# Kernel tuning notes

Hardware: AMD Instinct MI355X
Metric: run time of the kernel (lower is better)

The kernel has to match this reference:

```python
import jax, jax.numpy as jnp
import numpy as np

N = 50000      # nodes
E = 800000     # edges (avg degree 16)
DIN = 128
H = 128
DOUT = 64


def setup_inputs() -> dict:
    key = jax.random.key(0)
    ks = jax.random.split(key, 8)
    x = jax.random.normal(ks[0], (N, DIN), dtype=jnp.float32)
    edge_index = jax.random.randint(ks[1], (2, E), 0, N, dtype=jnp.int32)
    def glorot(k, fi, fo):
        return jax.random.normal(k, (fi, fo), dtype=jnp.float32) * (1.0 / np.sqrt(fi))
    return {
        "x": x,
        "edge_index": edge_index,
        "W1": glorot(ks[2], DIN, H), "b1": jnp.zeros((H,), jnp.float32),
        "W2": glorot(ks[3], H, H),   "b2": jnp.zeros((H,), jnp.float32),
        "W3": glorot(ks[4], H, DOUT),"b3": jnp.zeros((DOUT,), jnp.float32),
    }


def reference(x, edge_index, W1, b1, W2, b2, W3, b3):
    n = x.shape[0]
    # GCNConv: add self-loops, symmetric degree normalization D^-1/2 (A+I) D^-1/2
    loop = jnp.arange(n, dtype=edge_index.dtype)
    src = jnp.concatenate([edge_index[0], loop])  # [E+N]
    dst = jnp.concatenate([edge_index[1], loop])
    deg = jax.ops.segment_sum(jnp.ones(src.shape, x.dtype), dst, num_segments=n)
    dinv = jnp.where(deg > 0, jax.lax.rsqrt(deg), 0.0)
    norm = dinv[src] * dinv[dst]  # [E+N]

    def conv(h, W, b):
        h = h @ W                                   # [N, out]
        msg = h[src] * norm[:, None]                # gather + scale
        return jax.ops.segment_sum(msg, dst, num_segments=n) + b

    # gelu after every layer except the last (forward breaks before act)
    h = jax.nn.gelu(conv(x, W1, b1), approximate=False)
    h = jax.nn.gelu(conv(h, W2, b2), approximate=False)
    return conv(h, W3, b3)
```

## Files before the change

### kernel.cpp

```cpp
#include <hip/hip_runtime.h>
#include <math.h>

#define NDIN 128
#define NHID 128
#define NDOUT 64
#define NREP 8

typedef _Float16 half2_t __attribute__((ext_vector_type(2)));
typedef _Float16 half4_t __attribute__((ext_vector_type(4)));
typedef _Float16 half8_t __attribute__((ext_vector_type(8)));
typedef float    float4v __attribute__((ext_vector_type(4)));

__device__ __forceinline__ float gelu_exact(float x) {
    return 0.5f * x * (1.0f + erff(x * 0.70710678118654752f));
}


__device__ void wtrans_tile(const float* __restrict__ W, _Float16* __restrict__ Wt,
                            int K, int N, int bx, int by) {
    __shared__ float tile[32][33];
    int tx = threadIdx.x & 31, ty = threadIdx.x >> 5;
    for (int i = 0; i < 32; i += 8) {
        int k = by * 32 + ty + i, nn = bx * 32 + tx;
        tile[ty + i][tx] = (k < K && nn < N) ? W[(size_t)k * N + nn] : 0.f;
    }
    __syncthreads();
    for (int i = 0; i < 32; i += 8) {
        int nn = bx * 32 + ty + i, k = by * 32 + tx;
        if (nn < N && k < K) Wt[(size_t)nn * K + k] = (_Float16)tile[tx][ty + i];
    }
}

__global__ __launch_bounds__(256) void prep0_kernel(
    const float* __restrict__ W1, _Float16* __restrict__ W1t,
    const float* __restrict__ W2, _Float16* __restrict__ W2t,
    const float* __restrict__ W3, _Float16* __restrict__ W3t,
    int* __restrict__ countR, int* __restrict__ done, int n) {
    int b = blockIdx.x;
    if (b < 16) {
        wtrans_tile(W1, W1t, NDIN, NHID, b & 3, b >> 2);
    } else if (b < 32) {
        wtrans_tile(W2, W2t, NHID, NHID, (b - 16) & 3, (b - 16) >> 2);
    } else if (b < 40) {
        wtrans_tile(W3, W3t, NHID, NDOUT, (b - 32) & 1, (b - 32) >> 1);
    } else {
        int z = b - 40;
        int i = z * 256 + threadIdx.x;
        if (i < NREP * n) countR[i] = 0;
        if (z == 0 && threadIdx.x < 64) done[threadIdx.x] = 0;
    }
}


__global__ void count_kernel(const int* __restrict__ dst, int* __restrict__ countR,
                             int* __restrict__ eslot, int E, int n) {
    int b = blockIdx.x;
    int e = b * 256 + threadIdx.x;
    if (e < E) eslot[e] = atomicAdd(&countR[(b & (NREP - 1)) * n + dst[e]], 1);
}


__global__ __launch_bounds__(256) void reduce_scan_kernel(
    int* __restrict__ countR, int* __restrict__ blocksum, int* __restrict__ blockoff,
    int* __restrict__ rowptr, float* __restrict__ dinv, int* __restrict__ done,
    int nb, int n) {
    __shared__ int s[256];
    __shared__ int flag;
    __shared__ int boff_s;
    int t = threadIdx.x;
    int i = blockIdx.x * 256 + t;
    int deg = 0;
    if (i < n) {
        int pre = 0;
#pragma unroll
        for (int r = 0; r < NREP; r++) {
            int c = countR[r * n + i];
            countR[r * n + i] = pre;
            pre += c;
        }
        deg = pre;
    }
    s[t] = deg;
    __syncthreads();
    for (int off = 128; off > 0; off >>= 1) {
        if (t < off) s[t] += s[t + off];
        __syncthreads();
    }
    if (t == 0) {
        atomicExch(&blocksum[blockIdx.x], s[0]);
        __threadfence();
        int old = atomicAdd(&done[0], 1);
        flag = (old == nb - 1) ? 1 : 0;
    }
    __syncthreads();
    if (flag) {
        __threadfence();
        int pv = (t < nb) ? atomicAdd(&blocksum[t], 0) : 0;
        s[t] = pv;
        __syncthreads();
        for (int off = 1; off < 256; off <<= 1) {
            int u = (t >= off) ? s[t - off] : 0;
            __syncthreads();
            s[t] += u;
            __syncthreads();
        }
        if (t < nb) atomicExch(&blockoff[t], s[t] - pv);
        if (t == 255) rowptr[n] = s[255];
        __threadfence();
        if (t == 0) atomicExch(&done[1], 1);
    } else if (t == 0) {
        while (atomicAdd(&done[1], 0) == 0) __builtin_amdgcn_s_sleep(2);
        __threadfence();
    }
    __syncthreads();
    if (t == 0) boff_s = atomicAdd(&blockoff[blockIdx.x], 0);
    s[t] = deg;
    __syncthreads();
    for (int off = 1; off < 256; off <<= 1) {
        int u = (t >= off) ? s[t - off] : 0;
        __syncthreads();
        s[t] += u;
        __syncthreads();
    }
    if (i < n) {
        rowptr[i] = boff_s + s[t] - deg;
        dinv[i] = rsqrtf((float)(deg + 1));
    }
}


__global__ void fill_kernel(const int* __restrict__ src, const int* __restrict__ dst,
                            const int* __restrict__ eslot, const float* __restrict__ dinv,
                            const int* __restrict__ rowptr, const int* __restrict__ countR,
                            int2* __restrict__ adj, int E, int n) {
    int e = blockIdx.x * 256 + threadIdx.x;
    if (e >= E) return;
    int s = src[e], d = dst[e];
    int r = (e >> 8) & (NREP - 1);
    int p = rowptr[d] + countR[r * n + d] + eslot[e];
    adj[p] = make_int2(s, __float_as_int(dinv[s] * dinv[d]));
}


template <int BN, bool AF16>
__global__ __launch_bounds__(256) void gemm_mfma(
    const void* __restrict__ Aptr, const _Float16* __restrict__ Bt,
    _Float16* __restrict__ T, int M) {
    __shared__ _Float16 lds_a[64][136];
    __shared__ _Float16 lds_bt[BN][136];
    const int K = 128;
    int tid = threadIdx.x;
    int bm = blockIdx.x * 64;
    int wave = tid >> 6, lane = tid & 63;
    int m = lane & 15, quad = lane >> 4;

    if (AF16) {
        const _Float16* A = (const _Float16*)Aptr;
#pragma unroll
        for (int j = 0; j < 4; j++) {
            int c = tid + j * 256;
            int r = c >> 4, col = (c & 15) << 3;
            int grow = bm + r;
            uint4 v = make_uint4(0, 0, 0, 0);
            if (grow < M) v = *(const uint4*)(A + (size_t)grow * K + col);
            *(uint4*)&lds_a[r][col] = v;
        }
    } else {
        const float* A = (const float*)Aptr;
#pragma unroll
        for (int j = 0; j < 8; j++) {
            int c = tid + j * 256;
            int r = c >> 5, col = (c & 31) << 2;
            int grow = bm + r;
            float4 v = make_float4(0.f, 0.f, 0.f, 0.f);
            if (grow < M) v = *(const float4*)(A + (size_t)grow * K + col);
            half4_t h;
            h[0] = (_Float16)v.x; h[1] = (_Float16)v.y;
            h[2] = (_Float16)v.z; h[3] = (_Float16)v.w;
            *(half4_t*)&lds_a[r][col] = h;
        }
    }
    {
        const int chunks = BN * K / 8;
        for (int c = tid; c < chunks; c += 256) {
            int r = c >> 4, col = (c & 15) << 3;
            *(uint4*)&lds_bt[r][col] = *(const uint4*)(Bt + (size_t)r * K + col);
        }
    }
    __syncthreads();

    const int NT = BN / 16;
    float4v acc[NT];
#pragma unroll
    for (int nt = 0; nt < NT; nt++) acc[nt] = (float4v){0.f, 0.f, 0.f, 0.f};

    int arow = (wave << 4) + m;
#pragma unroll
    for (int kc = 0; kc < K; kc += 32) {
        half8_t a = *(const half8_t*)&lds_a[arow][kc + quad * 8];
#pragma unroll
        for (int nt = 0; nt < NT; nt++) {
            half8_t b = *(const half8_t*)&lds_bt[nt * 16 + m][kc + quad * 8];
            acc[nt] = __builtin_amdgcn_mfma_f32_16x16x32_f16(a, b, acc[nt], 0, 0, 0);
        }
    }
#pragma unroll
    for (int nt = 0; nt < NT; nt++) {
#pragma unroll
        for (int r = 0; r < 4; r++) {
            int grow = bm + (wave << 4) + (quad << 2) + r;
            if (grow < M) T[(size_t)grow * BN + nt * 16 + m] = (_Float16)acc[nt][r];
        }
    }
}


__device__ __forceinline__ half2_t agg_node128(
    const half2_t* __restrict__ t2, const int* __restrict__ rowptr,
    const int2* __restrict__ adj, const float* __restrict__ dinv,
    const float* __restrict__ bias, int node, int lane) {
    float wself = dinv[node];
    wself *= wself;
    half2_t v = t2[(size_t)node * 64 + lane];
    float accx = wself * (float)v[0], accy = wself * (float)v[1];
    int beg = rowptr[node], end = rowptr[node + 1];
    for (int e0 = beg; e0 < end; e0 += 64) {
        int rem = end - e0;
        int j = 0; float w = 0.f;
        if (lane < rem) {
            int2 ed = adj[e0 + lane];
            j = ed.x; w = __int_as_float(ed.y);
        }
        int cnt = rem < 64 ? rem : 64;
        for (int c = 0; c < cnt; c += 16) {
#pragma unroll
            for (int i = 0; i < 16; i++) {
                int jj = __builtin_amdgcn_readlane(j, c + i);
                float ww = __int_as_float(
                    __builtin_amdgcn_readlane(__float_as_int(w), c + i));
                half2_t u = t2[(size_t)jj * 64 + lane];
                accx += ww * (float)u[0];
                accy += ww * (float)u[1];
            }
        }
    }
    float2 b = ((const float2*)bias)[lane];
    accx = gelu_exact(accx + b.x);
    accy = gelu_exact(accy + b.y);
    half2_t o; o[0] = (_Float16)accx; o[1] = (_Float16)accy;
    return o;
}


template <int BN>
__global__ __launch_bounds__(256) void agg_gemm16_kernel(
    const _Float16* __restrict__ t, const int* __restrict__ rowptr,
    const int2* __restrict__ adj, const float* __restrict__ dinv,
    const float* __restrict__ bias, const _Float16* __restrict__ Bt,
    _Float16* __restrict__ T, int M) {
    __shared__ _Float16 lds_a[16][136];
    int tid = threadIdx.x;
    int wave = tid >> 6, lane = tid & 63;
    int bm = blockIdx.x * 16;
    const half2_t* t2 = (const half2_t*)t;
#pragma unroll 1
    for (int p = 0; p < 4; p++) {
        int r = (wave << 2) + p;
        int node = bm + r;
        half2_t o;
        o[0] = (_Float16)0.f; o[1] = (_Float16)0.f;
        if (node < M) o = agg_node128(t2, rowptr, adj, dinv, bias, node, lane);
        *(half2_t*)&lds_a[r][lane << 1] = o;
    }
    __syncthreads();

    int m = lane & 15, quad = lane >> 4;
    const int NT = BN / 64;
    float4v acc[NT];
#pragma unroll
    for (int nt = 0; nt < NT; nt++) acc[nt] = (float4v){0.f, 0.f, 0.f, 0.f};
#pragma unroll
    for (int kc = 0; kc < 128; kc += 32) {
        half8_t a = *(const half8_t*)&lds_a[m][kc + quad * 8];
#pragma unroll
        for (int nt = 0; nt < NT; nt++) {
            int col = wave * (BN / 4) + nt * 16 + m;
            half8_t b = *(const half8_t*)&Bt[(size_t)col * 128 + kc + quad * 8];
            acc[nt] = __builtin_amdgcn_mfma_f32_16x16x32_f16(a, b, acc[nt], 0, 0, 0);
        }
    }
#pragma unroll
    for (int nt = 0; nt < NT; nt++) {
#pragma unroll
        for (int r = 0; r < 4; r++) {
            int grow = bm + (quad << 2) + r;
            int col = wave * (BN / 4) + nt * 16 + m;
            if (grow < M) T[(size_t)grow * BN + col] = (_Float16)acc[nt][r];
        }
    }
}


template <int F, bool DOGELU, bool OUTF16>
__global__ __launch_bounds__(256) void agg_kernel(
    const _Float16* __restrict__ t, const int* __restrict__ rowptr,
    const int2* __restrict__ adj, const float* __restrict__ dinv,
    const float* __restrict__ bias, void* __restrict__ outp, int n) {
    int node = (int)((blockIdx.x * blockDim.x + threadIdx.x) >> 6);
    int lane = threadIdx.x & 63;
    if (node >= n) return;

    float wself = dinv[node];
    wself *= wself;
    int beg = rowptr[node];
    int end = rowptr[node + 1];

    if (F == 128) {
        const half2_t* t2 = (const half2_t*)t;
        half2_t v = t2[(size_t)node * 64 + lane];
        float accx = wself * (float)v[0], accy = wself * (float)v[1];
        for (int e0 = beg; e0 < end; e0 += 64) {
            int rem = end - e0;
            int j = 0; float w = 0.f;
            if (lane < rem) {
                int2 ed = adj[e0 + lane];
                j = ed.x; w = __int_as_float(ed.y);
            }
            int cnt = rem < 64 ? rem : 64;
            for (int c = 0; c < cnt; c += 16) {
#pragma unroll
                for (int i = 0; i < 16; i++) {
                    int jj = __builtin_amdgcn_readlane(j, c + i);
                    float ww = __int_as_float(
                        __builtin_amdgcn_readlane(__float_as_int(w), c + i));
                    half2_t u = t2[(size_t)jj * 64 + lane];
                    accx += ww * (float)u[0];
                    accy += ww * (float)u[1];
                }
            }
        }
        float2 b = ((const float2*)bias)[lane];
        accx += b.x; accy += b.y;
        if (DOGELU) { accx = gelu_exact(accx); accy = gelu_exact(accy); }
        if (OUTF16) {
            half2_t o; o[0] = (_Float16)accx; o[1] = (_Float16)accy;
            ((half2_t*)outp)[(size_t)node * 64 + lane] = o;
        } else {
            float2 o; o.x = accx; o.y = accy;
            ((float2*)outp)[(size_t)node * 64 + lane] = o;
        }
    } else {
        float acc = wself * (float)t[(size_t)node * 64 + lane];
        for (int e0 = beg; e0 < end; e0 += 64) {
            int rem = end - e0;
            int j = 0; float w = 0.f;
            if (lane < rem) {
                int2 ed = adj[e0 + lane];
                j = ed.x; w = __int_as_float(ed.y);
            }
            int cnt = rem < 64 ? rem : 64;
            for (int c = 0; c < cnt; c += 16) {
#pragma unroll
                for (int i = 0; i < 16; i++) {
                    int jj = __builtin_amdgcn_readlane(j, c + i);
                    float ww = __int_as_float(
                        __builtin_amdgcn_readlane(__float_as_int(w), c + i));
                    acc += ww * (float)t[(size_t)jj * 64 + lane];
                }
            }
        }
        acc += bias[lane];
        if (DOGELU) acc = gelu_exact(acc);
        if (OUTF16) ((_Float16*)outp)[(size_t)node * 64 + lane] = (_Float16)acc;
        else        ((float*)outp)[(size_t)node * 64 + lane] = acc;
    }
}


extern "C" void kernel_launch(void* const* d_in, const int* in_sizes, int n_in,
                              void* d_out, int out_size, void* d_ws, size_t ws_size,
                              hipStream_t stream) {
    const float* x  = (const float*)d_in[0];
    const int* edge = (const int*)d_in[1];
    const float* W1 = (const float*)d_in[2];
    const float* b1 = (const float*)d_in[3];
    const float* W2 = (const float*)d_in[4];
    const float* b2 = (const float*)d_in[5];
    const float* W3 = (const float*)d_in[6];
    const float* b3 = (const float*)d_in[7];
    float* out = (float*)d_out;

    const int N = in_sizes[0] / NDIN;
    const int E = in_sizes[1] / 2;
    const int* src = edge;
    const int* dst = edge + E;
    const int NB = (N + 255) / 256;
    const int NBZ = (NREP * N + 255) / 256;

    char* p = (char*)d_ws;
    auto alloc = [&](size_t bytes) {
        char* q = p;
        p += (bytes + 255) & ~(size_t)255;
        return q;
    };
    int*       countR   = (int*)alloc((size_t)NREP * N * 4);
    int*       rowptr   = (int*)alloc((size_t)(N + 1) * 4);
    int*       blocksum = (int*)alloc((size_t)NB * 4);
    int*       blockoff = (int*)alloc((size_t)NB * 4);
    int*       done     = (int*)alloc(256);
    float*     dinv     = (float*)alloc((size_t)N * 4);
    int*       eslot    = (int*)alloc((size_t)E * 4);
    int2*      adj      = (int2*)alloc((size_t)E * 8);
    _Float16*  W1t      = (_Float16*)alloc((size_t)NHID * NDIN * 2);
    _Float16*  W2t      = (_Float16*)alloc((size_t)NHID * NHID * 2);
    _Float16*  W3t      = (_Float16*)alloc((size_t)NDOUT * NHID * 2);
    _Float16*  tbuf     = (_Float16*)alloc((size_t)N * NHID * 2);
    _Float16*  hbuf     = (_Float16*)alloc((size_t)N * NHID * 2);

    dim3 blk(256);
    int mtiles = (N + 63) / 64;
    int ntiles16 = (N + 15) / 16;
    int eblocks = (E + 255) / 256;
    int agg_blocks = (N + 3) / 4;

    prep0_kernel<<<40 + NBZ, blk, 0, stream>>>(W1, W1t, W2, W2t, W3, W3t,
                                               countR, done, N);
    count_kernel<<<eblocks, blk, 0, stream>>>(dst, countR, eslot, E, N);
    gemm_mfma<128, false><<<mtiles, blk, 0, stream>>>(x, W1t, tbuf, N);
    reduce_scan_kernel<<<NB, blk, 0, stream>>>(countR, blocksum, blockoff, rowptr,
                                               dinv, done, NB, N);
    fill_kernel<<<eblocks, blk, 0, stream>>>(src, dst, eslot, dinv, rowptr, countR,
                                             adj, E, N);
    agg_gemm16_kernel<128><<<ntiles16, blk, 0, stream>>>(tbuf, rowptr, adj, dinv, b1,
                                                         W2t, hbuf, N);
    agg_gemm16_kernel<64><<<ntiles16, blk, 0, stream>>>(hbuf, rowptr, adj, dinv, b2,
                                                        W3t, tbuf, N);
    agg_kernel<64, false, false><<<agg_blocks, blk, 0, stream>>>(tbuf, rowptr, adj,
                                                                 dinv, b3, out, N);
}
```

Baseline: 269.0 us.

## Merge edge counting with first GEMM and unfuse aggregation from later GEMMs

Merges the edge-count kernel and the layer-1 GEMM into one launch, with block ranges split between atomic counting and MFMA GEMM tiles, so the two independent jobs can overlap. It also replaces the fused aggregate+GEMM kernels for layers 2 and 3 with separate agg_kernel and gemm_mfma launches. The fused kernels used small 16-row tiles and reread the weights per tile. The split version adds kernel launches and a round trip of the hidden activations through global memory.

```diff
diff --git a/kernel.cpp b/kernel.cpp
--- a/kernel.cpp
+++ b/kernel.cpp
@@ -52,11 +52,65 @@
 }
 
 
-__global__ void count_kernel(const int* __restrict__ dst, int* __restrict__ countR,
-                             int* __restrict__ eslot, int E, int n) {
+template <int BN>
+__device__ __forceinline__ void gemm_phaseB(
+    const _Float16 (*lds_a)[136], const _Float16* __restrict__ Bt,
+    _Float16* __restrict__ T, int bm, int M) {
+    int tid = threadIdx.x;
+    int wave = tid >> 6, lane = tid & 63;
+    int m = lane & 15, quad = lane >> 4;
+    const int NT = BN / 16;
+    float4v acc[NT];
+#pragma unroll
+    for (int nt = 0; nt < NT; nt++) acc[nt] = (float4v){0.f, 0.f, 0.f, 0.f};
+    int arow = (wave << 4) + m;
+#pragma unroll
+    for (int kc = 0; kc < 128; kc += 32) {
+        half8_t a = *(const half8_t*)&lds_a[arow][kc + quad * 8];
+#pragma unroll
+        for (int nt = 0; nt < NT; nt++) {
+            half8_t b = *(const half8_t*)&Bt[(size_t)(nt * 16 + m) * 128 + kc + quad * 8];
+            acc[nt] = __builtin_amdgcn_mfma_f32_16x16x32_f16(a, b, acc[nt], 0, 0, 0);
+        }
+    }
+#pragma unroll
+    for (int nt = 0; nt < NT; nt++) {
+#pragma unroll
+        for (int r = 0; r < 4; r++) {
+            int grow = bm + (wave << 4) + (quad << 2) + r;
+            if (grow < M) T[(size_t)grow * BN + nt * 16 + m] = (_Float16)acc[nt][r];
+        }
+    }
+}
+
+
+__global__ __launch_bounds__(256) void count_gemm1_kernel(
+    const int* __restrict__ dst, int* __restrict__ countR, int* __restrict__ eslot,
+    int E, int n, const float* __restrict__ x, const _Float16* __restrict__ W1t,
+    _Float16* __restrict__ T, int M, int cblocks) {
+    __shared__ _Float16 lds_a[64][136];
     int b = blockIdx.x;
-    int e = b * 256 + threadIdx.x;
-    if (e < E) eslot[e] = atomicAdd(&countR[(b & (NREP - 1)) * n + dst[e]], 1);
+    if (b < cblocks) {
+        int e = b * 256 + threadIdx.x;
+        if (e < E) eslot[e] = atomicAdd(&countR[(b & (NREP - 1)) * n + dst[e]], 1);
+        return;
+    }
+    int bm = (b - cblocks) * 64;
+    int tid = threadIdx.x;
+#pragma unroll
+    for (int j = 0; j < 8; j++) {
+        int c = tid + j * 256;
+        int r = c >> 5, col = (c & 31) << 2;
+        int grow = bm + r;
+        float4 v = make_float4(0.f, 0.f, 0.f, 0.f);
+        if (grow < M) v = *(const float4*)(x + (size_t)grow * 128 + col);
+        half4_t h;
+        h[0] = (_Float16)v.x; h[1] = (_Float16)v.y;
+        h[2] = (_Float16)v.z; h[3] = (_Float16)v.w;
+        *(half4_t*)&lds_a[r][col] = h;
+    }
+    __syncthreads();
+    gemm_phaseB<128>(lds_a, W1t, T, bm, M);
 }
 
 
@@ -210,92 +264,6 @@
         for (int r = 0; r < 4; r++) {
             int grow = bm + (wave << 4) + (quad << 2) + r;
             if (grow < M) T[(size_t)grow * BN + nt * 16 + m] = (_Float16)acc[nt][r];
-        }
-    }
-}
-
-
-__device__ __forceinline__ half2_t agg_node128(
-    const half2_t* __restrict__ t2, const int* __restrict__ rowptr,
-    const int2* __restrict__ adj, const float* __restrict__ dinv,
-    const float* __restrict__ bias, int node, int lane) {
-    float wself = dinv[node];
-    wself *= wself;
-    half2_t v = t2[(size_t)node * 64 + lane];
-    float accx = wself * (float)v[0], accy = wself * (float)v[1];
-    int beg = rowptr[node], end = rowptr[node + 1];
-    for (int e0 = beg; e0 < end; e0 += 64) {
-        int rem = end - e0;
-        int j = 0; float w = 0.f;
-        if (lane < rem) {
-            int2 ed = adj[e0 + lane];
-            j = ed.x; w = __int_as_float(ed.y);
-        }
-        int cnt = rem < 64 ? rem : 64;
-        for (int c = 0; c < cnt; c += 16) {
-#pragma unroll
-            for (int i = 0; i < 16; i++) {
-                int jj = __builtin_amdgcn_readlane(j, c + i);
-                float ww = __int_as_float(
-                    __builtin_amdgcn_readlane(__float_as_int(w), c + i));
-                half2_t u = t2[(size_t)jj * 64 + lane];
-                accx += ww * (float)u[0];
-                accy += ww * (float)u[1];
-            }
-        }
-    }
-    float2 b = ((const float2*)bias)[lane];
-    accx = gelu_exact(accx + b.x);
-    accy = gelu_exact(accy + b.y);
-    half2_t o; o[0] = (_Float16)accx; o[1] = (_Float16)accy;
-    return o;
-}
-
-
-template <int BN>
-__global__ __launch_bounds__(256) void agg_gemm16_kernel(
-    const _Float16* __restrict__ t, const int* __restrict__ rowptr,
-    const int2* __restrict__ adj, const float* __restrict__ dinv,
-    const float* __restrict__ bias, const _Float16* __restrict__ Bt,
-    _Float16* __restrict__ T, int M) {
-    __shared__ _Float16 lds_a[16][136];
-    int tid = threadIdx.x;
-    int wave = tid >> 6, lane = tid & 63;
-    int bm = blockIdx.x * 16;
-    const half2_t* t2 = (const half2_t*)t;
-#pragma unroll 1
-    for (int p = 0; p < 4; p++) {
-        int r = (wave << 2) + p;
-        int node = bm + r;
-        half2_t o;
-        o[0] = (_Float16)0.f; o[1] = (_Float16)0.f;
-        if (node < M) o = agg_node128(t2, rowptr, adj, dinv, bias, node, lane);
-        *(half2_t*)&lds_a[r][lane << 1] = o;
-    }
-    __syncthreads();
-
-    int m = lane & 15, quad = lane >> 4;
-    const int NT = BN / 64;
-    float4v acc[NT];
-#pragma unroll
-    for (int nt = 0; nt < NT; nt++) acc[nt] = (float4v){0.f, 0.f, 0.f, 0.f};
-#pragma unroll
-    for (int kc = 0; kc < 128; kc += 32) {
-        half8_t a = *(const half8_t*)&lds_a[m][kc + quad * 8];
-#pragma unroll
-        for (int nt = 0; nt < NT; nt++) {
-            int col = wave * (BN / 4) + nt * 16 + m;
-            half8_t b = *(const half8_t*)&Bt[(size_t)col * 128 + kc + quad * 8];
-            acc[nt] = __builtin_amdgcn_mfma_f32_16x16x32_f16(a, b, acc[nt], 0, 0, 0);
-        }
-    }
-#pragma unroll
-    for (int nt = 0; nt < NT; nt++) {
-#pragma unroll
-        for (int r = 0; r < 4; r++) {
-            int grow = bm + (quad << 2) + r;
-            int col = wave * (BN / 4) + nt * 16 + m;
-            if (grow < M) T[(size_t)grow * BN + col] = (_Float16)acc[nt][r];
         }
     }
 }
@@ -419,22 +387,23 @@
 
     dim3 blk(256);
     int mtiles = (N + 63) / 64;
-    int ntiles16 = (N + 15) / 16;
     int eblocks = (E + 255) / 256;
     int agg_blocks = (N + 3) / 4;
 
     prep0_kernel<<<40 + NBZ, blk, 0, stream>>>(W1, W1t, W2, W2t, W3, W3t,
                                                countR, done, N);
-    count_kernel<<<eblocks, blk, 0, stream>>>(dst, countR, eslot, E, N);
-    gemm_mfma<128, false><<<mtiles, blk, 0, stream>>>(x, W1t, tbuf, N);
+    count_gemm1_kernel<<<eblocks + mtiles, blk, 0, stream>>>(
+        dst, countR, eslot, E, N, x, W1t, tbuf, N, eblocks);
     reduce_scan_kernel<<<NB, blk, 0, stream>>>(countR, blocksum, blockoff, rowptr,
                                                dinv, done, NB, N);
     fill_kernel<<<eblocks, blk, 0, stream>>>(src, dst, eslot, dinv, rowptr, countR,
                                              adj, E, N);
-    agg_gemm16_kernel<128><<<ntiles16, blk, 0, stream>>>(tbuf, rowptr, adj, dinv, b1,
-                                                         W2t, hbuf, N);
-    agg_gemm16_kernel<64><<<ntiles16, blk, 0, stream>>>(hbuf, rowptr, adj, dinv, b2,
-                                                        W3t, tbuf, N);
+    agg_kernel<128, true, true><<<agg_blocks, blk, 0, stream>>>(tbuf, rowptr, adj,
+                                                                dinv, b1, hbuf, N);
+    gemm_mfma<128, true><<<mtiles, blk, 0, stream>>>(hbuf, W2t, tbuf, N);
+    agg_kernel<128, true, true><<<agg_blocks, blk, 0, stream>>>(tbuf, rowptr, adj,
+                                                                dinv, b2, hbuf, N);
+    gemm_mfma<64, true><<<mtiles, blk, 0, stream>>>(hbuf, W3t, tbuf, N);
     agg_kernel<64, false, false><<<agg_blocks, blk, 0, stream>>>(tbuf, rowptr, adj,
                                                                  dinv, b3, out, N);
 }
```

Measured after the change: 276.4 us. 2.7% more time.
